# Kernel optimization log

Measured on AMD Instinct MI355X. Metric: run time of the kernel, lower is better.

## Reference

```python
import jax, jax.numpy as jnp
import numpy as np

DIM = 768
HEADS = 12
HEAD_DIM = DIM // HEADS
SCALE = HEAD_DIM ** -0.5


def setup_inputs() -> dict:
    key = jax.random.key(0)
    ks = jax.random.split(key, 7)
    B, N, C = 4, 1024, DIM
    s = 0.02
    return {
        "x": jax.random.normal(ks[0], (B, N, C), dtype=jnp.float32),
        "attn_mask": jax.random.normal(ks[1], (B, N, N), dtype=jnp.float32) * 0.1,
        "w_qkv": jax.random.normal(ks[2], (3 * C, C), dtype=jnp.float32) * s,
        "w_proj": jax.random.normal(ks[3], (C, C), dtype=jnp.float32) * s,
        "b_proj": jnp.zeros((C,), dtype=jnp.float32),
        "w_pre": jax.random.normal(ks[4], (HEADS, HEADS), dtype=jnp.float32) * 0.2,
        "w_post": jax.random.normal(ks[5], (HEADS, HEADS), dtype=jnp.float32) * 0.2,
    }


def reference(x, attn_mask, w_qkv, w_proj, b_proj, w_pre, w_post):
    B, N, C = x.shape
    H, D = HEADS, HEAD_DIM
    qkv = (x @ w_qkv.T).reshape(B, N, 3, H, D)
    q, k, v = jnp.moveaxis(qkv, 2, 0)          # each [B, N, H, D]
    q = q.transpose(0, 2, 1, 3)                # [B, H, N, D]
    k = k.transpose(0, 2, 1, 3)
    v = v.transpose(0, 2, 1, 3)
    attn = jnp.einsum("bhnd,bhmd->bhnm", q, k) * SCALE
    attn = attn + attn_mask[:, None, :, :]
    # talking-heads pre-softmax mixing: Linear over head axis (y = x @ W.T)
    attn = jnp.einsum("bhnm,gh->bgnm", attn, w_pre)
    attn = jax.nn.softmax(attn, axis=-1)
    # talking-heads post-softmax mixing
    attn = jnp.einsum("bhnm,gh->bgnm", attn, w_post)
    out = jnp.einsum("bhnm,bhmd->bhnd", attn, v)   # [B, H, N, D]
    out = out.transpose(0, 2, 1, 3).reshape(B, N, C)
    return out @ w_proj.T + b_proj
```

## Files before the change

### kernel.cpp

```cpp
#include <hip/hip_runtime.h>
#include <hip/hip_bf16.h>

typedef __attribute__((ext_vector_type(8))) short bf16x8;
typedef __attribute__((ext_vector_type(4))) float f32x4;
typedef __attribute__((ext_vector_type(2))) float f32x2;
typedef unsigned short u16;
typedef unsigned int u32;

__device__ __forceinline__ u16 f2bf(float f){
  __hip_bfloat16 h = __float2bfloat16(f);
  return *reinterpret_cast<u16*>(&h);
}
__device__ __forceinline__ float bflo(u32 w){ return __uint_as_float(w << 16); }
__device__ __forceinline__ float bfhi(u32 w){ return __uint_as_float(w & 0xffff0000u); }

__device__ __forceinline__ void gload_lds16(const u16* g, u16* l){
  __builtin_amdgcn_global_load_lds(
      (__attribute__((address_space(1))) u32*)g,
      (__attribute__((address_space(3))) u32*)l, 16, 0, 0);
}

__global__ __launch_bounds__(256) void cvt3_kernel(
    const float* __restrict__ s0, u16* __restrict__ d0, int n0,
    const float* __restrict__ s1, u16* __restrict__ d1, int n1,
    const float* __restrict__ s2, u16* __restrict__ d2, int n2)
{
  int i = blockIdx.x*256 + threadIdx.x;
  const float* s; u16* d; int idx; float sc = 1.f;
  if (i < n0){ s = s0; d = d0; idx = i; }
  else if (i < n0 + n1){
    idx = i - n0; s = s1; d = d1;
    if (idx < 768*192) sc = 0.125f;
  } else if (i < n0 + n1 + n2){
    idx = i - n0 - n1; s = s2; d = d2;
  } else return;
  float4 v = reinterpret_cast<const float4*>(s)[idx];
  ushort4 o;
  o.x = f2bf(v.x*sc); o.y = f2bf(v.y*sc); o.z = f2bf(v.z*sc); o.w = f2bf(v.w*sc);
  reinterpret_cast<ushort4*>(d)[idx] = o;
}

template<int BM, int BN, int BK, int MODE>
__global__ __launch_bounds__(256) void gemm_bt(
    const u16* __restrict__ A, const u16* __restrict__ B,
    void* __restrict__ C0, void* __restrict__ C1, void* __restrict__ C2,
    const float* __restrict__ bias,
    int M, int N, int K, int lda, int ldb, long sA, long sB, long sC)
{
  constexpr int LDT = BK;
  constexpr int CB  = BK/8;
  __shared__ __align__(16) u16 As[BM*LDT];
  __shared__ __align__(16) u16 Bs[BN*LDT];
  const int z = blockIdx.z;
  const u16* Ab = A + (long)z * sA;
  const u16* Bb = B + (long)z * sB;
  const int bm = blockIdx.x * BM, bn = blockIdx.y * BN;
  const int tid = threadIdx.x, lane = tid & 63, wv = tid >> 6;
  constexpr int WM = BM/2, WN = BN/2, FM = WM/16, FN = WN/16;
  const int wm = (wv >> 1) * WM, wn = (wv & 1) * WN;
  const int quad = lane >> 4, cl = lane & 15;
  f32x4 acc[FM][FN];
  #pragma unroll
  for (int i=0;i<FM;i++)
    #pragma unroll
    for (int j=0;j<FN;j++){ f32x4 zr = {0.f,0.f,0.f,0.f}; acc[i][j] = zr; }
  constexpr int AIT = (BM*BK)/(8*256);
  constexpr int BIT = (BN*BK)/(8*256);

  for (int kb = 0; kb < K; kb += BK){
    __syncthreads();
    #pragma unroll
    for (int sL=0; sL<AIT; sL++){
      int e = tid + sL*256, r = e / CB, c8 = (e % CB) * 8;
      gload_lds16(Ab + (long)(bm + r)*lda + kb + c8, &As[e*8]);
    }
    #pragma unroll
    for (int sL=0; sL<BIT; sL++){
      int e = tid + sL*256, r = e / CB, c8 = (e % CB) * 8;
      gload_lds16(Bb + (long)(bn + r)*ldb + kb + c8, &Bs[e*8]);
    }
    __syncthreads();
    #pragma unroll
    for (int ks=0; ks<BK/32; ks++){
      bf16x8 af[FM], bfr[FN];
      #pragma unroll
      for (int i=0;i<FM;i++)
        af[i] = *reinterpret_cast<const bf16x8*>(&As[(wm + i*16 + cl)*LDT + ks*32 + quad*8]);
      #pragma unroll
      for (int j=0;j<FN;j++)
        bfr[j] = *reinterpret_cast<const bf16x8*>(&Bs[(wn + j*16 + cl)*LDT + ks*32 + quad*8]);
      #pragma unroll
      for (int i=0;i<FM;i++)
        #pragma unroll
        for (int j=0;j<FN;j++)
          acc[i][j] = __builtin_amdgcn_mfma_f32_16x16x32_bf16(af[i], bfr[j], acc[i][j], 0, 0, 0);
    }
  }

  #pragma unroll
  for (int i=0;i<FM;i++)
  #pragma unroll
  for (int j=0;j<FN;j++)
  #pragma unroll
  for (int r=0;r<4;r++){
    int gm = bm + wm + i*16 + quad*4 + r;
    int gn = bn + wn + j*16 + cl;
    float v = acc[i][j][r];
    if (MODE == 0){
      int b_ = gm >> 10, n_ = gm & 1023;
      int t3 = (gn >= 1536) ? 2 : ((gn >= 768) ? 1 : 0);
      int rem = gn - t3*768;
      int h = rem >> 6, d = rem & 63;
      u16 hv = f2bf(v);
      if (t3 == 0)      ((u16*)C0)[((long)((b_*12 + h)*1024 + n_))*64 + d] = hv;
      else if (t3 == 1) ((u16*)C1)[((long)((b_*12 + h)*1024 + n_))*64 + d] = hv;
      else              ((u16*)C2)[((long)((b_*12 + h)*64 + d))*1024 + n_] = hv;
    } else if (MODE == 1){
      ((u16*)C0)[(long)z*sC + (long)gm*N + gn] = f2bf(v);
    } else if (MODE == 2){
      int b_ = z / 12, h = z - b_*12;
      ((u16*)C0)[((long)((b_*1024 + gm)*12 + h))*64 + gn] = f2bf(v);
    } else {
      ((float*)C0)[(long)gm*N + gn] = v + bias[gn];
    }
  }
}

__global__ __launch_bounds__(256) void mix_kernel(
    u16* __restrict__ S, const float* __restrict__ mask,
    const float* __restrict__ w_pre, const float* __restrict__ w_post)
{
  const int bid = blockIdx.x;
  const int b = bid >> 10, n = bid & 1023;
  const int t = threadIdx.x;
  const int wv = t >> 6, lane = t & 63;
  const int m0 = t * 4;
  const long base0 = (((long)(b*12))*1024 + n) * 1024;

  uint2 raw[12];
  #pragma unroll
  for (int h=0; h<12; h++)
    raw[h] = *reinterpret_cast<const uint2*>(S + base0 + (long)h*1024*1024 + m0);
  float4 mk4 = *reinterpret_cast<const float4*>(mask + ((long)(b*1024 + n))*1024 + m0);

  f32x2 smix[12][2];
  {
    f32x2 mkA = {mk4.x, mk4.y}, mkB = {mk4.z, mk4.w};
    #pragma unroll
    for (int g=0; g<12; g++){
      float rs = 0.f;
      #pragma unroll
      for (int h=0; h<12; h++) rs += w_pre[g*12 + h];
      smix[g][0] = rs * mkA;
      smix[g][1] = rs * mkB;
    }
  }
  #pragma unroll
  for (int h=0; h<12; h++){
    f32x2 s0 = {bflo(raw[h].x), bfhi(raw[h].x)};
    f32x2 s1 = {bflo(raw[h].y), bfhi(raw[h].y)};
    #pragma unroll
    for (int g=0; g<12; g++){
      float w = w_pre[g*12 + h];
      smix[g][0] += w * s0;
      smix[g][1] += w * s1;
    }
  }

  __shared__ float redS[12][4];
  float L[12];
  #pragma unroll
  for (int g=0; g<12; g++){
    float e0 = __expf(smix[g][0][0]);
    float e1 = __expf(smix[g][0][1]);
    float e2 = __expf(smix[g][1][0]);
    float e3 = __expf(smix[g][1][1]);
    smix[g][0][0]=e0; smix[g][0][1]=e1; smix[g][1][0]=e2; smix[g][1][1]=e3;
    L[g] = (e0 + e1) + (e2 + e3);
  }
  #pragma unroll
  for (int off=32; off>0; off>>=1)
    #pragma unroll
    for (int g=0; g<12; g++) L[g] += __shfl_xor(L[g], off);
  if (lane == 0){
    #pragma unroll
    for (int g=0; g<12; g++) redS[g][wv] = L[g];
  }
  __syncthreads();
  #pragma unroll
  for (int g=0; g<12; g++){
    float Lt = (redS[g][0] + redS[g][1]) + (redS[g][2] + redS[g][3]);
    float inv;
    asm("v_rcp_f32 %0, %1" : "=v"(inv) : "v"(Lt));
    smix[g][0] *= inv;
    smix[g][1] *= inv;
  }

  #pragma unroll
  for (int h=0; h<12; h++){
    f32x2 o0, o1;
    {
      float w = w_post[h*12];
      o0 = w * smix[0][0];
      o1 = w * smix[0][1];
    }
    #pragma unroll
    for (int g=1; g<12; g++){
      float w = w_post[h*12 + g];
      o0 += w * smix[g][0];
      o1 += w * smix[g][1];
    }
    ushort4 st;
    st.x = f2bf(o0[0]); st.y = f2bf(o0[1]);
    st.z = f2bf(o1[0]); st.w = f2bf(o1[1]);
    *reinterpret_cast<ushort4*>(S + base0 + (long)h*1024*1024 + m0) = st;
  }
}

extern "C" void kernel_launch(void* const* d_in, const int* in_sizes, int n_in,
                              void* d_out, int out_size, void* d_ws, size_t ws_size,
                              hipStream_t stream)
{
  const float* x      = (const float*)d_in[0];
  const float* mask   = (const float*)d_in[1];
  const float* w_qkv  = (const float*)d_in[2];
  const float* w_proj = (const float*)d_in[3];
  const float* b_proj = (const float*)d_in[4];
  const float* w_pre  = (const float*)d_in[5];
  const float* w_post = (const float*)d_in[6];
  float* out = (float*)d_out;

  u16* xb     = (u16*)d_ws;
  u16* wqkvb  = xb     + 4096l*768;
  u16* wprojb = wqkvb  + 2304l*768;
  u16* Qb     = wprojb + 768l*768;
  u16* Kb     = Qb     + 48l*1024*64;
  u16* Vtb    = Kb     + 48l*1024*64;
  u16* tmpb   = Vtb    + 48l*1024*64;
  u16* Sb     = tmpb   + 4096l*768;
  size_t need = ((size_t)(Sb - xb) + 48ul*1024*1024) * sizeof(u16);
  if (ws_size < need) return;

  const int n0 = 4096*768/4, n1 = 2304*768/4, n2 = 768*768/4;
  cvt3_kernel<<<(n0+n1+n2 + 255)/256, 256, 0, stream>>>(x, xb, n0, w_qkv, wqkvb, n1,
                                                        w_proj, wprojb, n2);

  dim3 gq(4096/128, 2304/128, 1);
  gemm_bt<128,128,64,0><<<gq, 256, 0, stream>>>(xb, wqkvb, Qb, Kb, Vtb, nullptr,
      4096, 2304, 768, 768, 768, 0, 0, 0);

  dim3 gs(1024/128, 1024/128, 48);
  gemm_bt<128,128,64,1><<<gs, 256, 0, stream>>>(Qb, Kb, Sb, nullptr, nullptr, nullptr,
      1024, 1024, 64, 64, 64, 1024l*64, 1024l*64, 1024l*1024);

  mix_kernel<<<4096, 256, 0, stream>>>(Sb, mask, w_pre, w_post);

  dim3 gp(1024/128, 1, 48);
  gemm_bt<128,64,64,2><<<gp, 256, 0, stream>>>(Sb, Vtb, tmpb, nullptr, nullptr, nullptr,
      1024, 64, 1024, 1024, 1024, 1024l*1024, 64l*1024, 0);

  dim3 go(4096/128, 768/128, 1);
  gemm_bt<128,128,64,3><<<go, 256, 0, stream>>>(tmpb, wprojb, out, nullptr, nullptr, b_proj,
      4096, 768, 768, 768, 768, 0, 0, 0);
}
```

Before: 252.4 us.

## Shrink GEMM K-tiles, use exp2 in mix softmax, replace shuffle reduction with LDS

The K-tile depth of all four GEMMs drops from 64 to 32, and the PV GEMM moves to 64x64 tiles with twice as many blocks along M. In the mix kernel, the log2(e) factor is folded into the pre-mixing weights so the raw v_exp_f32 instruction can replace __expf. The 12-way wavefront shuffle reduction of row sums is replaced by a two-stage reduction through shared memory, which adds extra __syncthreads barriers. Smaller K tiles mean more loop iterations and barriers per GEMM, but less LDS per block and possibly higher occupancy.

```diff
diff --git a/kernel.cpp b/kernel.cpp
--- a/kernel.cpp
+++ b/kernel.cpp
@@ -133,9 +133,9 @@
   const int bid = blockIdx.x;
   const int b = bid >> 10, n = bid & 1023;
   const int t = threadIdx.x;
-  const int wv = t >> 6, lane = t & 63;
   const int m0 = t * 4;
   const long base0 = (((long)(b*12))*1024 + n) * 1024;
+  constexpr float LOG2E = 1.44269504f;
 
   uint2 raw[12];
   #pragma unroll
@@ -151,6 +151,7 @@
       float rs = 0.f;
       #pragma unroll
       for (int h=0; h<12; h++) rs += w_pre[g*12 + h];
+      rs *= LOG2E;
       smix[g][0] = rs * mkA;
       smix[g][1] = rs * mkB;
     }
@@ -161,37 +162,50 @@
     f32x2 s1 = {bflo(raw[h].y), bfhi(raw[h].y)};
     #pragma unroll
     for (int g=0; g<12; g++){
-      float w = w_pre[g*12 + h];
+      float w = w_pre[g*12 + h] * LOG2E;
       smix[g][0] += w * s0;
       smix[g][1] += w * s1;
     }
   }
 
-  __shared__ float redS[12][4];
   float L[12];
   #pragma unroll
   for (int g=0; g<12; g++){
-    float e0 = __expf(smix[g][0][0]);
-    float e1 = __expf(smix[g][0][1]);
-    float e2 = __expf(smix[g][1][0]);
-    float e3 = __expf(smix[g][1][1]);
+    float e0, e1, e2, e3;
+    asm("v_exp_f32 %0, %1" : "=v"(e0) : "v"(smix[g][0][0]));
+    asm("v_exp_f32 %0, %1" : "=v"(e1) : "v"(smix[g][0][1]));
+    asm("v_exp_f32 %0, %1" : "=v"(e2) : "v"(smix[g][1][0]));
+    asm("v_exp_f32 %0, %1" : "=v"(e3) : "v"(smix[g][1][1]));
     smix[g][0][0]=e0; smix[g][0][1]=e1; smix[g][1][0]=e2; smix[g][1][1]=e3;
     L[g] = (e0 + e1) + (e2 + e3);
   }
-  #pragma unroll
-  for (int off=32; off>0; off>>=1)
-    #pragma unroll
-    for (int g=0; g<12; g++) L[g] += __shfl_xor(L[g], off);
-  if (lane == 0){
-    #pragma unroll
-    for (int g=0; g<12; g++) redS[g][wv] = L[g];
-  }
+
+  __shared__ float Lbuf[256*13];
+  __shared__ float Lseg[12*16];
+  __shared__ float invS[12];
+  #pragma unroll
+  for (int g=0; g<12; g++) Lbuf[t*13 + g] = L[g];
   __syncthreads();
+  if (t < 192){
+    int g = t >> 4, seg = t & 15;
+    float s = 0.f;
+    #pragma unroll
+    for (int i=0; i<16; i++) s += Lbuf[(seg*16 + i)*13 + g];
+    Lseg[g*16 + seg] = s;
+  }
+  __syncthreads();
+  if (t < 12){
+    float s = 0.f;
+    #pragma unroll
+    for (int i=0; i<16; i++) s += Lseg[t*16 + i];
+    float inv;
+    asm("v_rcp_f32 %0, %1" : "=v"(inv) : "v"(s));
+    invS[t] = inv;
+  }
+  __syncthreads();
   #pragma unroll
   for (int g=0; g<12; g++){
-    float Lt = (redS[g][0] + redS[g][1]) + (redS[g][2] + redS[g][3]);
-    float inv;
-    asm("v_rcp_f32 %0, %1" : "=v"(inv) : "v"(Lt));
+    float inv = invS[g];
     smix[g][0] *= inv;
     smix[g][1] *= inv;
   }
@@ -246,20 +260,20 @@
                                                         w_proj, wprojb, n2);
 
   dim3 gq(4096/128, 2304/128, 1);
-  gemm_bt<128,128,64,0><<<gq, 256, 0, stream>>>(xb, wqkvb, Qb, Kb, Vtb, nullptr,
+  gemm_bt<128,128,32,0><<<gq, 256, 0, stream>>>(xb, wqkvb, Qb, Kb, Vtb, nullptr,
       4096, 2304, 768, 768, 768, 0, 0, 0);
 
   dim3 gs(1024/128, 1024/128, 48);
-  gemm_bt<128,128,64,1><<<gs, 256, 0, stream>>>(Qb, Kb, Sb, nullptr, nullptr, nullptr,
+  gemm_bt<128,128,32,1><<<gs, 256, 0, stream>>>(Qb, Kb, Sb, nullptr, nullptr, nullptr,
       1024, 1024, 64, 64, 64, 1024l*64, 1024l*64, 1024l*1024);
 
   mix_kernel<<<4096, 256, 0, stream>>>(Sb, mask, w_pre, w_post);
 
-  dim3 gp(1024/128, 1, 48);
-  gemm_bt<128,64,64,2><<<gp, 256, 0, stream>>>(Sb, Vtb, tmpb, nullptr, nullptr, nullptr,
+  dim3 gp(1024/64, 1, 48);
+  gemm_bt<64,64,32,2><<<gp, 256, 0, stream>>>(Sb, Vtb, tmpb, nullptr, nullptr, nullptr,
       1024, 64, 1024, 1024, 1024, 1024l*1024, 64l*1024, 0);
 
   dim3 go(4096/128, 768/128, 1);
-  gemm_bt<128,128,64,3><<<go, 256, 0, stream>>>(tmpb, wprojb, out, nullptr, nullptr, b_proj,
+  gemm_bt<128,128,32,3><<<go, 256, 0, stream>>>(tmpb, wprojb, out, nullptr, nullptr, b_proj,
       4096, 768, 768, 768, 768, 0, 0, 0);
 }
```

Result: faster. 244.2 us (-3.3%).

## Use packed bf16 conversion, exp2 softmax, and shrink GEMM K-tile to 32

Applied to the files above, without the earlier changes.

Replaces scalar bf16 conversions with the packed v_cvt_pk_bf16_f32 instruction in the convert and mix kernels. It folds log2(e) into the pre-mix weights so the softmax can call v_exp_f32 directly, avoiding the scaling that __expf adds. It also cuts the K tile of every GEMM from 64 to 32, which halves LDS per block and may raise occupancy, at the cost of more loop iterations and more barriers. The hidden GEMM body must handle BK=32 correctly, and the change from round-to-nearest to hardware rounding in the conversion can alter the result slightly.

```diff
diff --git a/kernel.cpp b/kernel.cpp
--- a/kernel.cpp
+++ b/kernel.cpp
@@ -13,6 +13,11 @@
 }
 __device__ __forceinline__ float bflo(u32 w){ return __uint_as_float(w << 16); }
 __device__ __forceinline__ float bfhi(u32 w){ return __uint_as_float(w & 0xffff0000u); }
+__device__ __forceinline__ u32 pack2bf(float a, float b){
+  u32 r;
+  asm("v_cvt_pk_bf16_f32 %0, %1, %2" : "=v"(r) : "v"(a), "v"(b));
+  return r;
+}
 
 __device__ __forceinline__ void gload_lds16(const u16* g, u16* l){
   __builtin_amdgcn_global_load_lds(
@@ -35,9 +40,10 @@
     idx = i - n0 - n1; s = s2; d = d2;
   } else return;
   float4 v = reinterpret_cast<const float4*>(s)[idx];
-  ushort4 o;
-  o.x = f2bf(v.x*sc); o.y = f2bf(v.y*sc); o.z = f2bf(v.z*sc); o.w = f2bf(v.w*sc);
-  reinterpret_cast<ushort4*>(d)[idx] = o;
+  uint2 o;
+  o.x = pack2bf(v.x*sc, v.y*sc);
+  o.y = pack2bf(v.z*sc, v.w*sc);
+  reinterpret_cast<uint2*>(d)[idx] = o;
 }
 
 template<int BM, int BN, int BK, int MODE>
@@ -136,6 +142,7 @@
   const int wv = t >> 6, lane = t & 63;
   const int m0 = t * 4;
   const long base0 = (((long)(b*12))*1024 + n) * 1024;
+  constexpr float LOG2E = 1.44269504f;
 
   uint2 raw[12];
   #pragma unroll
@@ -151,6 +158,7 @@
       float rs = 0.f;
       #pragma unroll
       for (int h=0; h<12; h++) rs += w_pre[g*12 + h];
+      rs *= LOG2E;
       smix[g][0] = rs * mkA;
       smix[g][1] = rs * mkB;
     }
@@ -161,7 +169,7 @@
     f32x2 s1 = {bflo(raw[h].y), bfhi(raw[h].y)};
     #pragma unroll
     for (int g=0; g<12; g++){
-      float w = w_pre[g*12 + h];
+      float w = w_pre[g*12 + h] * LOG2E;
       smix[g][0] += w * s0;
       smix[g][1] += w * s1;
     }
@@ -171,10 +179,11 @@
   float L[12];
   #pragma unroll
   for (int g=0; g<12; g++){
-    float e0 = __expf(smix[g][0][0]);
-    float e1 = __expf(smix[g][0][1]);
-    float e2 = __expf(smix[g][1][0]);
-    float e3 = __expf(smix[g][1][1]);
+    float e0, e1, e2, e3;
+    asm("v_exp_f32 %0, %1" : "=v"(e0) : "v"(smix[g][0][0]));
+    asm("v_exp_f32 %0, %1" : "=v"(e1) : "v"(smix[g][0][1]));
+    asm("v_exp_f32 %0, %1" : "=v"(e2) : "v"(smix[g][1][0]));
+    asm("v_exp_f32 %0, %1" : "=v"(e3) : "v"(smix[g][1][1]));
     smix[g][0][0]=e0; smix[g][0][1]=e1; smix[g][1][0]=e2; smix[g][1][1]=e3;
     L[g] = (e0 + e1) + (e2 + e3);
   }
@@ -210,10 +219,10 @@
       o0 += w * smix[g][0];
       o1 += w * smix[g][1];
     }
-    ushort4 st;
-    st.x = f2bf(o0[0]); st.y = f2bf(o0[1]);
-    st.z = f2bf(o1[0]); st.w = f2bf(o1[1]);
-    *reinterpret_cast<ushort4*>(S + base0 + (long)h*1024*1024 + m0) = st;
+    uint2 st;
+    st.x = pack2bf(o0[0], o0[1]);
+    st.y = pack2bf(o1[0], o1[1]);
+    *reinterpret_cast<uint2*>(S + base0 + (long)h*1024*1024 + m0) = st;
   }
 }
 
@@ -246,20 +255,20 @@
                                                         w_proj, wprojb, n2);
 
   dim3 gq(4096/128, 2304/128, 1);
-  gemm_bt<128,128,64,0><<<gq, 256, 0, stream>>>(xb, wqkvb, Qb, Kb, Vtb, nullptr,
+  gemm_bt<128,128,32,0><<<gq, 256, 0, stream>>>(xb, wqkvb, Qb, Kb, Vtb, nullptr,
       4096, 2304, 768, 768, 768, 0, 0, 0);
 
   dim3 gs(1024/128, 1024/128, 48);
-  gemm_bt<128,128,64,1><<<gs, 256, 0, stream>>>(Qb, Kb, Sb, nullptr, nullptr, nullptr,
+  gemm_bt<128,128,32,1><<<gs, 256, 0, stream>>>(Qb, Kb, Sb, nullptr, nullptr, nullptr,
       1024, 1024, 64, 64, 64, 1024l*64, 1024l*64, 1024l*1024);
 
   mix_kernel<<<4096, 256, 0, stream>>>(Sb, mask, w_pre, w_post);
 
   dim3 gp(1024/128, 1, 48);
-  gemm_bt<128,64,64,2><<<gp, 256, 0, stream>>>(Sb, Vtb, tmpb, nullptr, nullptr, nullptr,
+  gemm_bt<128,64,32,2><<<gp, 256, 0, stream>>>(Sb, Vtb, tmpb, nullptr, nullptr, nullptr,
       1024, 64, 1024, 1024, 1024, 1024l*1024, 64l*1024, 0);
 
   dim3 go(4096/128, 768/128, 1);
-  gemm_bt<128,128,64,3><<<go, 256, 0, stream>>>(tmpb, wprojb, out, nullptr, nullptr, b_proj,
+  gemm_bt<128,128,32,3><<<go, 256, 0, stream>>>(tmpb, wprojb, out, nullptr, nullptr, b_proj,
       4096, 768, 768, 768, 768, 0, 0, 0);
 }
```

After: 248.9 us. Within noise of the previous version (-1.4%).
